# Performance work log

Hardware: AMD Instinct MI355X
Metric: run time of the kernel (lower is better)

Reference implementation:

```python
import jax, jax.numpy as jnp
import numpy as np

B, INP, H, DH = 8192, 2048, 8, 256
HD = H * DH            # 2048
PROJ = int(4 / 3 * HD)  # 2731
EPS = 1e-5


def _layernorm(x, w, b):
    mu = jnp.mean(x, axis=-1, keepdims=True)
    var = jnp.mean((x - mu) ** 2, axis=-1, keepdims=True)
    return (x - mu) * jax.lax.rsqrt(var + EPS) * w + b


def _groupnorm(x, w, b):
    # x: [B, HD] -> groups of size DH (one group per head)
    xg = x.reshape(-1, H, DH)
    mu = jnp.mean(xg, axis=-1, keepdims=True)
    var = jnp.mean((xg - mu) ** 2, axis=-1, keepdims=True)
    xn = ((xg - mu) * jax.lax.rsqrt(var + EPS)).reshape(-1, HD)
    return xn * w + b


def _block_linear(h, R):
    # h: [B, HD], R: [H, DH, DH] block-diagonal recurrent weights (no bias)
    hh = h.reshape(-1, H, DH)
    return jnp.einsum('bhd,hde->bhe', hh, R).reshape(-1, HD)


def setup_inputs() -> dict:
    key = jax.random.key(0)
    ks = jax.random.split(key, 16)
    s = 0.02
    return {
        'seq': jax.random.normal(ks[0], (B, INP), jnp.float32),
        'c_tm1': jnp.zeros((B, HD), jnp.float32),
        'n_tm1': jnp.ones((B, HD), jnp.float32),
        'h_tm1': jnp.zeros((B, HD), jnp.float32),
        'm_tm1': jnp.zeros((B, HD), jnp.float32),
        'ln_w': jnp.ones((INP,), jnp.float32),
        'ln_b': jnp.zeros((INP,), jnp.float32),
        'gn_w': jnp.ones((HD,), jnp.float32),
        'gn_b': jnp.zeros((HD,), jnp.float32),
        'W_i': jax.random.normal(ks[1], (INP, HD), jnp.float32) * s,
        'b_i': jnp.zeros((HD,), jnp.float32),
        'W_f': jax.random.normal(ks[2], (INP, HD), jnp.float32) * s,
        'b_f': jnp.zeros((HD,), jnp.float32),
        'W_z': jax.random.normal(ks[3], (INP, HD), jnp.float32) * s,
        'b_z': jnp.zeros((HD,), jnp.float32),
        'W_o': jax.random.normal(ks[4], (INP, HD), jnp.float32) * s,
        'b_o': jnp.zeros((HD,), jnp.float32),
        'R_i': jax.random.normal(ks[5], (H, DH, DH), jnp.float32) * s,
        'R_f': jax.random.normal(ks[6], (H, DH, DH), jnp.float32) * s,
        'R_z': jax.random.normal(ks[7], (H, DH, DH), jnp.float32) * s,
        'R_o': jax.random.normal(ks[8], (H, DH, DH), jnp.float32) * s,
        'W_up': jax.random.normal(ks[9], (HD, 2 * PROJ), jnp.float32) * s,
        'b_up': jnp.zeros((2 * PROJ,), jnp.float32),
        'W_dn': jax.random.normal(ks[10], (PROJ, INP), jnp.float32) * s,
        'b_dn': jnp.zeros((INP,), jnp.float32),
    }


def reference(seq, c_tm1, n_tm1, h_tm1, m_tm1, ln_w, ln_b, gn_w, gn_b,
              W_i, b_i, W_f, b_f, W_z, b_z, W_o, b_o,
              R_i, R_f, R_z, R_o, W_up, b_up, W_dn, b_dn):
    x_t = _layernorm(seq, ln_w, ln_b)
    x_c = x_t  # use_conv=False path

    i_t = x_c @ W_i + b_i + _block_linear(h_tm1, R_i)
    f_t = x_c @ W_f + b_f + _block_linear(h_tm1, R_f)
    z_t = x_t @ W_z + b_z + _block_linear(h_tm1, R_z)
    o_t = x_t @ W_o + b_o + _block_linear(h_tm1, R_o)

    m_t = jnp.maximum(f_t + m_tm1, i_t)          # stabilizer state
    i_g = jnp.exp(i_t - m_t)
    f_g = jnp.exp(f_t - m_t + m_tm1)
    z_g = jnp.tanh(z_t)
    o_g = jax.nn.sigmoid(o_t)

    c_t = f_g * c_tm1 + i_g * z_g
    n_t = f_g * n_tm1 + i_g
    h_t = o_g * (c_t / n_t)

    out = _groupnorm(h_t, gn_w, gn_b)
    up = out @ W_up + b_up
    out1, out2 = up[:, :PROJ], up[:, PROJ:]
    out = out1 + jax.nn.gelu(out2, approximate=False)
    out = out @ W_dn + b_dn
    return (out + seq, (c_t, n_t, h_t, m_t))
```

## Files before the change

### kernel.cpp

```cpp
#include <hip/hip_runtime.h>
#include <math.h>

typedef unsigned short u16;
typedef __attribute__((ext_vector_type(4))) float f32x4;
typedef __attribute__((ext_vector_type(8))) short bf16x8;
typedef __attribute__((ext_vector_type(8))) unsigned short u16x8;

#define B_ROWS 8192
#define GLDS(gaddr, laddr)                                                                  \
  __builtin_amdgcn_global_load_lds(                                                        \
      (const __attribute__((address_space(1))) unsigned int*)(const void*)(gaddr),          \
      (__attribute__((address_space(3))) unsigned int*)(void*)(laddr), 16, 0, 0)

__device__ __forceinline__ u16 f2bf(float f) {
  unsigned int u = __float_as_uint(f);
  unsigned int r = u + 0x7fffu + ((u >> 16) & 1u);
  return (u16)(r >> 16);
}

__device__ __forceinline__ bf16x8 dsr(unsigned a) {
  bf16x8 d;
  asm volatile("ds_read_b128 %0, %1" : "=v"(d) : "v"(a));
  return d;
}

__device__ __forceinline__ void block_reduce2(float& a, float& b) {
  __shared__ float sb[8];
  #pragma unroll
  for (int off = 32; off > 0; off >>= 1) {
    a += __shfl_down(a, off, 64);
    b += __shfl_down(b, off, 64);
  }
  int lane = threadIdx.x & 63, wid = threadIdx.x >> 6;
  if (lane == 0) { sb[wid] = a; sb[wid + 4] = b; }
  __syncthreads();
  a = sb[0] + sb[1] + sb[2] + sb[3];
  b = sb[4] + sb[5] + sb[6] + sb[7];
  __syncthreads();
}

__global__ __launch_bounds__(256) void ln_kernel(const float* __restrict__ seq,
                                                 const float* __restrict__ w,
                                                 const float* __restrict__ b,
                                                 u16* __restrict__ xbf) {
  int row = blockIdx.x, t = threadIdx.x;
  const f32x4* x = (const f32x4*)(seq + (size_t)row * 2048);
  f32x4 v0 = x[2 * t], v1 = x[2 * t + 1];
  float s = 0.f, q = 0.f;
  #pragma unroll
  for (int i = 0; i < 4; ++i) { s += v0[i] + v1[i]; q += v0[i] * v0[i] + v1[i] * v1[i]; }
  block_reduce2(s, q);
  float mu = s * (1.f / 2048.f);
  float var = q * (1.f / 2048.f) - mu * mu;
  float rstd = rsqrtf(var + 1e-5f);
  f32x4 w0 = ((const f32x4*)w)[2 * t], w1 = ((const f32x4*)w)[2 * t + 1];
  f32x4 b0 = ((const f32x4*)b)[2 * t], b1 = ((const f32x4*)b)[2 * t + 1];
  u16x8 o;
  #pragma unroll
  for (int i = 0; i < 4; ++i) o[i] = f2bf((v0[i] - mu) * rstd * w0[i] + b0[i]);
  #pragma unroll
  for (int i = 0; i < 4; ++i) o[4 + i] = f2bf((v1[i] - mu) * rstd * w1[i] + b1[i]);
  ((u16x8*)(xbf + (size_t)row * 2048))[t] = o;
}

__global__ __launch_bounds__(256) void cvt_bf16(const float* __restrict__ in,
                                                u16* __restrict__ out, int n) {
  int i = blockIdx.x * 256 + threadIdx.x;
  int stride = gridDim.x * 256;
  for (; i < n; i += stride) out[i] = f2bf(in[i]);
}

__global__ void transpose_cvt(const float* __restrict__ in, long ibstride, int R, int Cc,
                              u16* __restrict__ out, long obstride, int ldo) {
  in += (size_t)blockIdx.z * ibstride;
  out += (size_t)blockIdx.z * obstride;
  __shared__ float tile[32][33];
  int c0 = blockIdx.x * 32, r0 = blockIdx.y * 32;
  int tx = threadIdx.x, ty = threadIdx.y;
  #pragma unroll
  for (int j = 0; j < 4; ++j) {
    int rr = r0 + ty + j * 8;
    if (rr < R && c0 + tx < Cc) tile[ty + j * 8][tx] = in[(size_t)rr * Cc + c0 + tx];
  }
  __syncthreads();
  #pragma unroll
  for (int j = 0; j < 4; ++j) {
    int cc = c0 + ty + j * 8, rr = r0 + tx;
    if (cc < Cc && rr < R) out[(size_t)cc * ldo + rr] = f2bf(tile[tx][ty + j * 8]);
  }
}

__global__ __launch_bounds__(256) void pack_bias(const float* __restrict__ bi, const float* __restrict__ bf_,
                                                 const float* __restrict__ bz, const float* __restrict__ bo,
                                                 const float* __restrict__ bup,
                                                 float* __restrict__ biasg, float* __restrict__ biasup) {
  int i = blockIdx.x * 256 + threadIdx.x;
  if (i < 8192) {
    int g = i >> 11, j = i & 2047;
    const float* p = (g == 0) ? bi : (g == 1) ? bf_ : (g == 2) ? bz : bo;
    biasg[i] = p[j];
  }
  if (i < 5504) biasup[i] = (i < 5460) ? bup[i] : 0.f;
}

#define MFMA_CLUSTER(lo, AV, BV)                                                           \
  __builtin_amdgcn_s_setprio(1);                                                           \
  _Pragma("unroll")                                                                        \
  for (int mi = 0; mi < 4; ++mi)                                                           \
    _Pragma("unroll")                                                                      \
    for (int ni = 0; ni < 4; ++ni)                                                         \
      acc[(lo) + mi][ni] =                                                                 \
          __builtin_amdgcn_mfma_f32_16x16x32_bf16(AV[mi], BV[ni], acc[(lo) + mi][ni], 0, 0, 0); \
  __builtin_amdgcn_s_setprio(0);

#define WAIT_LGKM(N)                                                                       \
  asm volatile("s_waitcnt lgkmcnt(" #N ")" ::: "memory");                                  \
  __builtin_amdgcn_sched_barrier(0);

template<int REC>
__global__ __launch_bounds__(512, 2) void gemm256(
    const u16* __restrict__ A, int lda,
    const u16* __restrict__ Bt, int ldb, int KT,
    float* __restrict__ C, long ldc, int Nvalid, int ntN,
    const float* __restrict__ bias,
    const float* __restrict__ addsrc, int ldadd,
    const u16* __restrict__ hbf, const u16* __restrict__ RTw) {
  __shared__ __align__(16) u16 Al[2][2][256][32];
  __shared__ __align__(16) u16 Bl[2][2][256][32];
  const int NT = KT + (REC ? 4 : 0);

  int nb = gridDim.x;
  int bid = blockIdx.x;
  int per = nb >> 3;
  int id = (bid & 7) * per + (bid >> 3);
  int m0 = (id / ntN) * 256, n0 = (id % ntN) * 256;

  int tid = threadIdx.x, lane = tid & 63, wave = tid >> 6;
  int wm = wave >> 2, wn = wave & 3;
  int r = lane & 15, sgrp = lane >> 4;

  const u16* rsrc = nullptr; int hcol = 0;
  if (REC) {
    int g = n0 >> 11, head = (n0 & 2047) >> 8;
    rsrc = RTw + ((size_t)(g * 8 + head)) * 65536;
    hcol = head * 256;
  }

  auto stage = [&](int tt, int which) {
    if (tt >= NT) return;
    const int isA = (which < 2), kh = which & 1, slot = tt & 1;
    const u16* src; size_t ld;
    if (!REC || tt < KT) {
      if (isA) { src = A + (size_t)m0 * lda + tt * 64; ld = lda; }
      else     { src = Bt + (size_t)n0 * ldb + tt * 64; ld = ldb; }
    } else {
      int t2 = tt - KT;
      if (isA) { src = hbf + (size_t)m0 * 2048 + hcol + t2 * 64; ld = 2048; }
      else     { src = rsrc + t2 * 64; ld = 256; }
    }
    u16* base = isA ? &Al[slot][kh][0][0] : &Bl[slot][kh][0][0];
    #pragma unroll
    for (int c = 0; c < 2; ++c) {
      int R0 = wave * 32 + c * 16;
      int row = R0 + (lane >> 2);
      int s = (lane & 3) ^ ((row >> 1) & 3);
      GLDS(src + (size_t)row * ld + kh * 32 + s * 8, base + R0 * 32);
    }
  };

  unsigned AlB = (unsigned)(size_t)(__attribute__((address_space(3))) u16*)&Al[0][0][0][0];
  unsigned BlB = (unsigned)(size_t)(__attribute__((address_space(3))) u16*)&Bl[0][0][0][0];
  int sA = sgrp ^ ((r >> 1) & 3);
  unsigned aBaseT = AlB + (unsigned)((wm * 128 + r) * 64 + sA * 16);
  unsigned bBaseT = BlB + (unsigned)((wn * 64 + r) * 64 + sA * 16);

  f32x4 acc[8][4] = {};
  bf16x8 a0[4], a1[4], a2[4], a3[4], b0[4], b1[4];

  stage(0, 0); stage(0, 2); stage(0, 1); stage(0, 3);
  stage(1, 0); stage(1, 2);
  asm volatile("s_waitcnt vmcnt(4)" ::: "memory");
  __builtin_amdgcn_s_barrier();

  for (int t = 0; t < NT; ++t) {
    unsigned sl = (unsigned)(t & 1) * 32768u;
    unsigned ab = aBaseT + sl, bb = bBaseT + sl;
    __builtin_amdgcn_sched_barrier(0);
    a0[0] = dsr(ab);          a0[1] = dsr(ab + 1024);
    a0[2] = dsr(ab + 2048);   a0[3] = dsr(ab + 3072);
    b0[0] = dsr(bb);          b0[1] = dsr(bb + 1024);
    b0[2] = dsr(bb + 2048);   b0[3] = dsr(bb + 3072);
    a1[0] = dsr(ab + 4096);   a1[1] = dsr(ab + 5120);
    a1[2] = dsr(ab + 6144);   a1[3] = dsr(ab + 7168);
    stage(t + 1, 1); stage(t + 1, 3);
    WAIT_LGKM(4);
    MFMA_CLUSTER(0, a0, b0);
    a2[0] = dsr(ab + 16384);  a2[1] = dsr(ab + 17408);
    a2[2] = dsr(ab + 18432);  a2[3] = dsr(ab + 19456);
    b1[0] = dsr(bb + 16384);  b1[1] = dsr(bb + 17408);
    b1[2] = dsr(bb + 18432);  b1[3] = dsr(bb + 19456);
    WAIT_LGKM(8);
    MFMA_CLUSTER(4, a1, b0);
    __builtin_amdgcn_s_barrier();
    __builtin_amdgcn_sched_barrier(0);
    stage(t + 2, 0); stage(t + 2, 2);
    a3[0] = dsr(ab + 20480);  a3[1] = dsr(ab + 21504);
    a3[2] = dsr(ab + 22528);  a3[3] = dsr(ab + 23552);
    WAIT_LGKM(4);
    MFMA_CLUSTER(0, a2, b1);
    WAIT_LGKM(0);
    MFMA_CLUSTER(4, a3, b1);
    if (t + 2 < NT)      { asm volatile("s_waitcnt vmcnt(4)" ::: "memory"); }
    else if (t + 1 < NT) { asm volatile("s_waitcnt vmcnt(0)" ::: "memory"); }
    __builtin_amdgcn_s_barrier();
  }

  #pragma unroll
  for (int a = 0; a < 8; ++a) {
    int row0 = m0 + wm * 128 + a * 16 + sgrp * 4;
    #pragma unroll
    for (int ni = 0; ni < 4; ++ni) {
      int col = n0 + wn * 64 + ni * 16 + r;
      if (col >= Nvalid) continue;
      float bv = bias ? bias[col] : 0.f;
      #pragma unroll
      for (int jj = 0; jj < 4; ++jj) {
        float v = acc[a][ni][jj] + bv;
        if (addsrc) v += addsrc[(size_t)(row0 + jj) * ldadd + col];
        C[(size_t)(row0 + jj) * ldc + col] = v;
      }
    }
  }
}

__global__ __launch_bounds__(256) void pointwise_gn(
    const float* __restrict__ G, const float* __restrict__ c1, const float* __restrict__ n1,
    const float* __restrict__ m1, const float* __restrict__ gnw, const float* __restrict__ gnb,
    float* __restrict__ outc, float* __restrict__ outn, float* __restrict__ outh,
    float* __restrict__ outm, u16* __restrict__ gnbf) {
  int b = blockIdx.x >> 3, h = blockIdx.x & 7, t = threadIdx.x;
  int j = (h << 8) + t;
  size_t rg = (size_t)b * 8192;
  float it = G[rg + j], ft = G[rg + 2048 + j], zt = G[rg + 4096 + j], ot = G[rg + 6144 + j];
  size_t idx = (size_t)b * 2048 + j;
  float cp = c1[idx], np = n1[idx], mp = m1[idx];
  float mt = fmaxf(ft + mp, it);
  float ig = expf(it - mt), fg = expf(ft - mt + mp);
  float zg = tanhf(zt), og = 1.f / (1.f + expf(-ot));
  float ct = fg * cp + ig * zg;
  float nt = fg * np + ig;
  float ht = og * (ct / nt);
  outc[idx] = ct; outn[idx] = nt; outh[idx] = ht; outm[idx] = mt;
  float s = ht, q = ht * ht;
  block_reduce2(s, q);
  float mu = s * (1.f / 256.f);
  float var = q * (1.f / 256.f) - mu * mu;
  float xn = (ht - mu) * rsqrtf(var + 1e-5f);
  gnbf[idx] = f2bf(xn * gnw[j] + gnb[j]);
}

__global__ __launch_bounds__(256) void act_gelu(const float* __restrict__ tmp, u16* __restrict__ gl) {
  int b = blockIdx.x;
  const float* row = tmp + (size_t)b * 5504;
  u16* orow = gl + (size_t)b * 2752;
  for (int p = threadIdx.x; p < 2752; p += 256) {
    float y = 0.f;
    if (p < 2730) {
      float x1 = row[p], x2 = row[2730 + p];
      y = x1 + x2 * 0.5f * (1.f + erff(x2 * 0.70710678118f));
    }
    orow[p] = f2bf(y);
  }
}

extern "C" void kernel_launch(void* const* d_in, const int* in_sizes, int n_in,
                              void* d_out, int out_size, void* d_ws, size_t ws_size,
                              hipStream_t stream) {
  (void)in_sizes; (void)n_in; (void)out_size; (void)ws_size;
  const float* seq = (const float*)d_in[0];
  const float* c1  = (const float*)d_in[1];
  const float* n1  = (const float*)d_in[2];
  const float* h1  = (const float*)d_in[3];
  const float* m1  = (const float*)d_in[4];
  const float* lnw = (const float*)d_in[5];
  const float* lnb = (const float*)d_in[6];
  const float* gnw = (const float*)d_in[7];
  const float* gnb = (const float*)d_in[8];
  const float* Wi = (const float*)d_in[9];  const float* bi  = (const float*)d_in[10];
  const float* Wf = (const float*)d_in[11]; const float* bf_ = (const float*)d_in[12];
  const float* Wz = (const float*)d_in[13]; const float* bz  = (const float*)d_in[14];
  const float* Wo = (const float*)d_in[15]; const float* bo  = (const float*)d_in[16];
  const float* Ri = (const float*)d_in[17]; const float* Rf = (const float*)d_in[18];
  const float* Rz = (const float*)d_in[19]; const float* Ro = (const float*)d_in[20];
  const float* Wup = (const float*)d_in[21]; const float* bup = (const float*)d_in[22];
  const float* Wdn = (const float*)d_in[23]; const float* bdn = (const float*)d_in[24];

  size_t off = 0;
  char* base = (char*)d_ws;
  auto alloc = [&](size_t bytes) { char* p = base + off; off += (bytes + 255) & ~(size_t)255; return p; };
  u16*   XBF    = (u16*)  alloc((size_t)B_ROWS * 2048 * 2);
  u16*   HBF    = (u16*)  alloc((size_t)B_ROWS * 2048 * 2);
  u16*   WGT    = (u16*)  alloc((size_t)4 * 2048 * 2048 * 2);
  u16*   RT     = (u16*)  alloc((size_t)4 * 8 * 256 * 256 * 2);
  u16*   WUPT   = (u16*)  alloc((size_t)5632 * 2048 * 2);
  u16*   WDNT   = (u16*)  alloc((size_t)2048 * 2752 * 2);
  float* BIASG  = (float*)alloc((size_t)8192 * 4);
  float* BIASUP = (float*)alloc((size_t)5504 * 4);
  u16*   GNBF   = (u16*)  alloc((size_t)B_ROWS * 2048 * 2);
  float* G      = (float*)alloc((size_t)B_ROWS * 8192 * 4);
  float* TMP    = G;
  u16*   GL     = WGT;

  float* OUT  = (float*)d_out;
  float* OUTC = OUT + (size_t)B_ROWS * 2048;
  float* OUTN = OUTC + (size_t)B_ROWS * 2048;
  float* OUTH = OUTN + (size_t)B_ROWS * 2048;
  float* OUTM = OUTH + (size_t)B_ROWS * 2048;

  dim3 tb32(32, 8);

  ln_kernel<<<B_ROWS, 256, 0, stream>>>(seq, lnw, lnb, XBF);
  cvt_bf16<<<2048, 256, 0, stream>>>(h1, HBF, B_ROWS * 2048);
  transpose_cvt<<<dim3(64, 64, 1), tb32, 0, stream>>>(Wi, 0, 2048, 2048, WGT + (size_t)0 * 4194304, 0, 2048);
  transpose_cvt<<<dim3(64, 64, 1), tb32, 0, stream>>>(Wf, 0, 2048, 2048, WGT + (size_t)1 * 4194304, 0, 2048);
  transpose_cvt<<<dim3(64, 64, 1), tb32, 0, stream>>>(Wz, 0, 2048, 2048, WGT + (size_t)2 * 4194304, 0, 2048);
  transpose_cvt<<<dim3(64, 64, 1), tb32, 0, stream>>>(Wo, 0, 2048, 2048, WGT + (size_t)3 * 4194304, 0, 2048);
  transpose_cvt<<<dim3(8, 8, 8), tb32, 0, stream>>>(Ri, 65536, 256, 256, RT + (size_t)0 * 524288, 65536, 256);
  transpose_cvt<<<dim3(8, 8, 8), tb32, 0, stream>>>(Rf, 65536, 256, 256, RT + (size_t)1 * 524288, 65536, 256);
  transpose_cvt<<<dim3(8, 8, 8), tb32, 0, stream>>>(Rz, 65536, 256, 256, RT + (size_t)2 * 524288, 65536, 256);
  transpose_cvt<<<dim3(8, 8, 8), tb32, 0, stream>>>(Ro, 65536, 256, 256, RT + (size_t)3 * 524288, 65536, 256);
  transpose_cvt<<<dim3(171, 64, 1), tb32, 0, stream>>>(Wup, 0, 2048, 5460, WUPT, 0, 2048);
  transpose_cvt<<<dim3(64, 86, 1), tb32, 0, stream>>>(Wdn, 0, 2730, 2048, WDNT, 0, 2752);
  pack_bias<<<32, 256, 0, stream>>>(bi, bf_, bz, bo, bup, BIASG, BIASUP);
  gemm256<1><<<32 * 32, 512, 0, stream>>>(XBF, 2048, WGT, 2048, 32,
                                          G, 8192, 8192, 32, BIASG, nullptr, 0, HBF, RT);
  pointwise_gn<<<B_ROWS * 8, 256, 0, stream>>>(G, c1, n1, m1, gnw, gnb,
                                               OUTC, OUTN, OUTH, OUTM, GNBF);
  gemm256<0><<<32 * 22, 512, 0, stream>>>(GNBF, 2048, WUPT, 2048, 32,
                                          TMP, 5504, 5460, 22, BIASUP, nullptr, 0, nullptr, nullptr);
  act_gelu<<<8192, 256, 0, stream>>>(TMP, GL);
  gemm256<0><<<32 * 8, 512, 0, stream>>>(GL, 2752, WDNT, 2752, 43,
                                         OUT, 2048, 2048, 8, bdn, seq, 2048, nullptr, nullptr);
}
```

Baseline: 1.487 ms.

## Merge prep kernels, store up-proj in bf16, vectorize pointwise, reorder GEMM LDS loads

Combines the layernorm and h-to-bf16 conversion into one launch, and batches the gate and recurrent weight transposes into single launches. The up-projection GEMM now writes bf16 instead of fp32, which halves the intermediate traffic read by the GELU kernel. The pointwise/groupnorm kernel is vectorized to one row per block with wave-level reductions, and the main GEMM loop issues its global staging earlier and batches more LDS reads before the first MFMA cluster. Rounding the up-projection output to bf16 adds some precision loss ahead of GELU.

Result: no change. 1.490 ms (+0.2%).

```diff
diff --git a/kernel.cpp b/kernel.cpp
--- a/kernel.cpp
+++ b/kernel.cpp
@@ -5,6 +5,7 @@
 typedef __attribute__((ext_vector_type(4))) float f32x4;
 typedef __attribute__((ext_vector_type(8))) short bf16x8;
 typedef __attribute__((ext_vector_type(8))) unsigned short u16x8;
+typedef __attribute__((ext_vector_type(4))) unsigned short u16x4;
 
 #define B_ROWS 8192
 #define GLDS(gaddr, laddr)                                                                  \
@@ -16,6 +17,9 @@
   unsigned int u = __float_as_uint(f);
   unsigned int r = u + 0x7fffu + ((u >> 16) & 1u);
   return (u16)(r >> 16);
+}
+__device__ __forceinline__ float bf2f(u16 v) {
+  return __uint_as_float(((unsigned)v) << 16);
 }
 
 __device__ __forceinline__ bf16x8 dsr(unsigned a) {
@@ -39,41 +43,47 @@
   __syncthreads();
 }
 
-__global__ __launch_bounds__(256) void ln_kernel(const float* __restrict__ seq,
-                                                 const float* __restrict__ w,
-                                                 const float* __restrict__ b,
-                                                 u16* __restrict__ xbf) {
-  int row = blockIdx.x, t = threadIdx.x;
-  const f32x4* x = (const f32x4*)(seq + (size_t)row * 2048);
-  f32x4 v0 = x[2 * t], v1 = x[2 * t + 1];
-  float s = 0.f, q = 0.f;
-  #pragma unroll
-  for (int i = 0; i < 4; ++i) { s += v0[i] + v1[i]; q += v0[i] * v0[i] + v1[i] * v1[i]; }
-  block_reduce2(s, q);
-  float mu = s * (1.f / 2048.f);
-  float var = q * (1.f / 2048.f) - mu * mu;
-  float rstd = rsqrtf(var + 1e-5f);
-  f32x4 w0 = ((const f32x4*)w)[2 * t], w1 = ((const f32x4*)w)[2 * t + 1];
-  f32x4 b0 = ((const f32x4*)b)[2 * t], b1 = ((const f32x4*)b)[2 * t + 1];
-  u16x8 o;
-  #pragma unroll
-  for (int i = 0; i < 4; ++i) o[i] = f2bf((v0[i] - mu) * rstd * w0[i] + b0[i]);
-  #pragma unroll
-  for (int i = 0; i < 4; ++i) o[4 + i] = f2bf((v1[i] - mu) * rstd * w1[i] + b1[i]);
-  ((u16x8*)(xbf + (size_t)row * 2048))[t] = o;
-}
-
-__global__ __launch_bounds__(256) void cvt_bf16(const float* __restrict__ in,
-                                                u16* __restrict__ out, int n) {
-  int i = blockIdx.x * 256 + threadIdx.x;
-  int stride = gridDim.x * 256;
-  for (; i < n; i += stride) out[i] = f2bf(in[i]);
-}
-
-__global__ void transpose_cvt(const float* __restrict__ in, long ibstride, int R, int Cc,
-                              u16* __restrict__ out, long obstride, int ldo) {
-  in += (size_t)blockIdx.z * ibstride;
-  out += (size_t)blockIdx.z * obstride;
+__global__ __launch_bounds__(256) void ln_cvt(const float* __restrict__ seq,
+                                              const float* __restrict__ w,
+                                              const float* __restrict__ b,
+                                              u16* __restrict__ xbf,
+                                              const float* __restrict__ h1,
+                                              u16* __restrict__ hbf) {
+  if (blockIdx.x < 8192) {
+    int row = blockIdx.x, t = threadIdx.x;
+    const f32x4* x = (const f32x4*)(seq + (size_t)row * 2048);
+    f32x4 v0 = x[2 * t], v1 = x[2 * t + 1];
+    float s = 0.f, q = 0.f;
+    #pragma unroll
+    for (int i = 0; i < 4; ++i) { s += v0[i] + v1[i]; q += v0[i] * v0[i] + v1[i] * v1[i]; }
+    block_reduce2(s, q);
+    float mu = s * (1.f / 2048.f);
+    float var = q * (1.f / 2048.f) - mu * mu;
+    float rstd = rsqrtf(var + 1e-5f);
+    f32x4 w0 = ((const f32x4*)w)[2 * t], w1 = ((const f32x4*)w)[2 * t + 1];
+    f32x4 b0 = ((const f32x4*)b)[2 * t], b1 = ((const f32x4*)b)[2 * t + 1];
+    u16x8 o;
+    #pragma unroll
+    for (int i = 0; i < 4; ++i) o[i] = f2bf((v0[i] - mu) * rstd * w0[i] + b0[i]);
+    #pragma unroll
+    for (int i = 0; i < 4; ++i) o[4 + i] = f2bf((v1[i] - mu) * rstd * w1[i] + b1[i]);
+    ((u16x8*)(xbf + (size_t)row * 2048))[t] = o;
+  } else {
+    int chunk = blockIdx.x - 8192;
+    const f32x4* src = (const f32x4*)(h1 + (size_t)chunk * 8192);
+    u16x8* dst = (u16x8*)(hbf + (size_t)chunk * 8192);
+    for (int i = threadIdx.x; i < 1024; i += 256) {
+      f32x4 v0 = src[2 * i], v1 = src[2 * i + 1];
+      u16x8 o;
+      #pragma unroll
+      for (int j = 0; j < 4; ++j) { o[j] = f2bf(v0[j]); o[4 + j] = f2bf(v1[j]); }
+      dst[i] = o;
+    }
+  }
+}
+
+__device__ __forceinline__ void tr_tile(const float* in, int R, int Cc,
+                                        u16* out, int ldo) {
   __shared__ float tile[32][33];
   int c0 = blockIdx.x * 32, r0 = blockIdx.y * 32;
   int tx = threadIdx.x, ty = threadIdx.y;
@@ -88,6 +98,27 @@
     int cc = c0 + ty + j * 8, rr = r0 + tx;
     if (cc < Cc && rr < R) out[(size_t)cc * ldo + rr] = f2bf(tile[tx][ty + j * 8]);
   }
+}
+
+__global__ void transpose_cvt(const float* __restrict__ in, int R, int Cc,
+                              u16* __restrict__ out, int ldo) {
+  tr_tile(in, R, Cc, out, ldo);
+}
+
+__global__ void transpose_gate4(const float* __restrict__ W0, const float* __restrict__ W1,
+                                const float* __restrict__ W2, const float* __restrict__ W3,
+                                u16* __restrict__ out) {
+  int z = blockIdx.z;
+  const float* in = (z == 0) ? W0 : (z == 1) ? W1 : (z == 2) ? W2 : W3;
+  tr_tile(in, 2048, 2048, out + (size_t)z * 4194304, 2048);
+}
+
+__global__ void transpose_rec4(const float* __restrict__ R0, const float* __restrict__ R1,
+                               const float* __restrict__ R2, const float* __restrict__ R3,
+                               u16* __restrict__ out) {
+  int g = blockIdx.z >> 3, hd = blockIdx.z & 7;
+  const float* in = ((g == 0) ? R0 : (g == 1) ? R1 : (g == 2) ? R2 : R3) + (size_t)hd * 65536;
+  tr_tile(in, 256, 256, out + (size_t)g * 524288 + (size_t)hd * 65536, 256);
 }
 
 __global__ __launch_bounds__(256) void pack_bias(const float* __restrict__ bi, const float* __restrict__ bf_,
@@ -117,11 +148,11 @@
   asm volatile("s_waitcnt lgkmcnt(" #N ")" ::: "memory");                                  \
   __builtin_amdgcn_sched_barrier(0);
 
-template<int REC>
+template<int REC, int OB>
 __global__ __launch_bounds__(512, 2) void gemm256(
     const u16* __restrict__ A, int lda,
     const u16* __restrict__ Bt, int ldb, int KT,
-    float* __restrict__ C, long ldc, int Nvalid, int ntN,
+    void* __restrict__ Cv, long ldc, int Nvalid, int ntN,
     const float* __restrict__ bias,
     const float* __restrict__ addsrc, int ldadd,
     const u16* __restrict__ hbf, const u16* __restrict__ RTw) {
@@ -186,19 +217,19 @@
     unsigned sl = (unsigned)(t & 1) * 32768u;
     unsigned ab = aBaseT + sl, bb = bBaseT + sl;
     __builtin_amdgcn_sched_barrier(0);
+    stage(t + 1, 1); stage(t + 1, 3);
     a0[0] = dsr(ab);          a0[1] = dsr(ab + 1024);
     a0[2] = dsr(ab + 2048);   a0[3] = dsr(ab + 3072);
     b0[0] = dsr(bb);          b0[1] = dsr(bb + 1024);
     b0[2] = dsr(bb + 2048);   b0[3] = dsr(bb + 3072);
     a1[0] = dsr(ab + 4096);   a1[1] = dsr(ab + 5120);
     a1[2] = dsr(ab + 6144);   a1[3] = dsr(ab + 7168);
-    stage(t + 1, 1); stage(t + 1, 3);
-    WAIT_LGKM(4);
-    MFMA_CLUSTER(0, a0, b0);
     a2[0] = dsr(ab + 16384);  a2[1] = dsr(ab + 17408);
     a2[2] = dsr(ab + 18432);  a2[3] = dsr(ab + 19456);
     b1[0] = dsr(bb + 16384);  b1[1] = dsr(bb + 17408);
     b1[2] = dsr(bb + 18432);  b1[3] = dsr(bb + 19456);
+    WAIT_LGKM(12);
+    MFMA_CLUSTER(0, a0, b0);
     WAIT_LGKM(8);
     MFMA_CLUSTER(4, a1, b0);
     __builtin_amdgcn_s_barrier();
@@ -227,49 +258,76 @@
       for (int jj = 0; jj < 4; ++jj) {
         float v = acc[a][ni][jj] + bv;
         if (addsrc) v += addsrc[(size_t)(row0 + jj) * ldadd + col];
-        C[(size_t)(row0 + jj) * ldc + col] = v;
+        if (OB) ((u16*)Cv)[(size_t)(row0 + jj) * ldc + col] = f2bf(v);
+        else    ((float*)Cv)[(size_t)(row0 + jj) * ldc + col] = v;
       }
     }
   }
 }
 
-__global__ __launch_bounds__(256) void pointwise_gn(
+__global__ __launch_bounds__(512) void pointwise_gn(
     const float* __restrict__ G, const float* __restrict__ c1, const float* __restrict__ n1,
     const float* __restrict__ m1, const float* __restrict__ gnw, const float* __restrict__ gnb,
     float* __restrict__ outc, float* __restrict__ outn, float* __restrict__ outh,
     float* __restrict__ outm, u16* __restrict__ gnbf) {
-  int b = blockIdx.x >> 3, h = blockIdx.x & 7, t = threadIdx.x;
-  int j = (h << 8) + t;
+  int b = blockIdx.x;
+  int w = threadIdx.x >> 6, l = threadIdx.x & 63;
+  int j = (w << 8) + l * 4;
   size_t rg = (size_t)b * 8192;
-  float it = G[rg + j], ft = G[rg + 2048 + j], zt = G[rg + 4096 + j], ot = G[rg + 6144 + j];
+  f32x4 it = *(const f32x4*)(G + rg + j);
+  f32x4 ft = *(const f32x4*)(G + rg + 2048 + j);
+  f32x4 zt = *(const f32x4*)(G + rg + 4096 + j);
+  f32x4 ot = *(const f32x4*)(G + rg + 6144 + j);
   size_t idx = (size_t)b * 2048 + j;
-  float cp = c1[idx], np = n1[idx], mp = m1[idx];
-  float mt = fmaxf(ft + mp, it);
-  float ig = expf(it - mt), fg = expf(ft - mt + mp);
-  float zg = tanhf(zt), og = 1.f / (1.f + expf(-ot));
-  float ct = fg * cp + ig * zg;
-  float nt = fg * np + ig;
-  float ht = og * (ct / nt);
-  outc[idx] = ct; outn[idx] = nt; outh[idx] = ht; outm[idx] = mt;
-  float s = ht, q = ht * ht;
-  block_reduce2(s, q);
+  f32x4 cp = *(const f32x4*)(c1 + idx);
+  f32x4 np = *(const f32x4*)(n1 + idx);
+  f32x4 mp = *(const f32x4*)(m1 + idx);
+  f32x4 ct, nt, ht, mt;
+  float s = 0.f, q = 0.f;
+  #pragma unroll
+  for (int i = 0; i < 4; ++i) {
+    float m_ = fmaxf(ft[i] + mp[i], it[i]);
+    float ig = expf(it[i] - m_), fg = expf(ft[i] - m_ + mp[i]);
+    float zg = tanhf(zt[i]), og = 1.f / (1.f + expf(-ot[i]));
+    ct[i] = fg * cp[i] + ig * zg;
+    nt[i] = fg * np[i] + ig;
+    ht[i] = og * (ct[i] / nt[i]);
+    mt[i] = m_;
+    s += ht[i]; q += ht[i] * ht[i];
+  }
+  *(f32x4*)(outc + idx) = ct;
+  *(f32x4*)(outn + idx) = nt;
+  *(f32x4*)(outh + idx) = ht;
+  *(f32x4*)(outm + idx) = mt;
+  #pragma unroll
+  for (int off = 32; off > 0; off >>= 1) {
+    s += __shfl_xor(s, off, 64);
+    q += __shfl_xor(q, off, 64);
+  }
   float mu = s * (1.f / 256.f);
   float var = q * (1.f / 256.f) - mu * mu;
-  float xn = (ht - mu) * rsqrtf(var + 1e-5f);
-  gnbf[idx] = f2bf(xn * gnw[j] + gnb[j]);
-}
-
-__global__ __launch_bounds__(256) void act_gelu(const float* __restrict__ tmp, u16* __restrict__ gl) {
+  float rs = rsqrtf(var + 1e-5f);
+  f32x4 gw = *(const f32x4*)(gnw + j), gb = *(const f32x4*)(gnb + j);
+  u16x4 o;
+  #pragma unroll
+  for (int i = 0; i < 4; ++i) o[i] = f2bf((ht[i] - mu) * rs * gw[i] + gb[i]);
+  *(u16x4*)(gnbf + idx) = o;
+}
+
+__global__ __launch_bounds__(256) void act_gelu(const u16* __restrict__ tmp, u16* __restrict__ gl) {
   int b = blockIdx.x;
-  const float* row = tmp + (size_t)b * 5504;
+  const u16* row = tmp + (size_t)b * 5504;
   u16* orow = gl + (size_t)b * 2752;
-  for (int p = threadIdx.x; p < 2752; p += 256) {
-    float y = 0.f;
+  for (int p = threadIdx.x * 2; p < 2752; p += 512) {
+    float y0 = 0.f, y1 = 0.f;
     if (p < 2730) {
-      float x1 = row[p], x2 = row[2730 + p];
-      y = x1 + x2 * 0.5f * (1.f + erff(x2 * 0.70710678118f));
-    }
-    orow[p] = f2bf(y);
+      float x10 = bf2f(row[p]), x11 = bf2f(row[p + 1]);
+      float x20 = bf2f(row[2730 + p]), x21 = bf2f(row[2731 + p]);
+      y0 = x10 + x20 * 0.5f * (1.f + erff(x20 * 0.70710678118f));
+      y1 = x11 + x21 * 0.5f * (1.f + erff(x21 * 0.70710678118f));
+    }
+    orow[p] = f2bf(y0);
+    orow[p + 1] = f2bf(y1);
   }
 }
 
@@ -308,7 +366,7 @@
   float* BIASUP = (float*)alloc((size_t)5504 * 4);
   u16*   GNBF   = (u16*)  alloc((size_t)B_ROWS * 2048 * 2);
   float* G      = (float*)alloc((size_t)B_ROWS * 8192 * 4);
-  float* TMP    = G;
+  u16*   TMP    = (u16*)G;
   u16*   GL     = WGT;
 
   float* OUT  = (float*)d_out;
@@ -319,26 +377,19 @@
 
   dim3 tb32(32, 8);
 
-  ln_kernel<<<B_ROWS, 256, 0, stream>>>(seq, lnw, lnb, XBF);
-  cvt_bf16<<<2048, 256, 0, stream>>>(h1, HBF, B_ROWS * 2048);
-  transpose_cvt<<<dim3(64, 64, 1), tb32, 0, stream>>>(Wi, 0, 2048, 2048, WGT + (size_t)0 * 4194304, 0, 2048);
-  transpose_cvt<<<dim3(64, 64, 1), tb32, 0, stream>>>(Wf, 0, 2048, 2048, WGT + (size_t)1 * 4194304, 0, 2048);
-  transpose_cvt<<<dim3(64, 64, 1), tb32, 0, stream>>>(Wz, 0, 2048, 2048, WGT + (size_t)2 * 4194304, 0, 2048);
-  transpose_cvt<<<dim3(64, 64, 1), tb32, 0, stream>>>(Wo, 0, 2048, 2048, WGT + (size_t)3 * 4194304, 0, 2048);
-  transpose_cvt<<<dim3(8, 8, 8), tb32, 0, stream>>>(Ri, 65536, 256, 256, RT + (size_t)0 * 524288, 65536, 256);
-  transpose_cvt<<<dim3(8, 8, 8), tb32, 0, stream>>>(Rf, 65536, 256, 256, RT + (size_t)1 * 524288, 65536, 256);
-  transpose_cvt<<<dim3(8, 8, 8), tb32, 0, stream>>>(Rz, 65536, 256, 256, RT + (size_t)2 * 524288, 65536, 256);
-  transpose_cvt<<<dim3(8, 8, 8), tb32, 0, stream>>>(Ro, 65536, 256, 256, RT + (size_t)3 * 524288, 65536, 256);
-  transpose_cvt<<<dim3(171, 64, 1), tb32, 0, stream>>>(Wup, 0, 2048, 5460, WUPT, 0, 2048);
-  transpose_cvt<<<dim3(64, 86, 1), tb32, 0, stream>>>(Wdn, 0, 2730, 2048, WDNT, 0, 2752);
+  ln_cvt<<<8192 + 2048, 256, 0, stream>>>(seq, lnw, lnb, XBF, h1, HBF);
+  transpose_gate4<<<dim3(64, 64, 4), tb32, 0, stream>>>(Wi, Wf, Wz, Wo, WGT);
+  transpose_rec4<<<dim3(8, 8, 32), tb32, 0, stream>>>(Ri, Rf, Rz, Ro, RT);
+  transpose_cvt<<<dim3(171, 64, 1), tb32, 0, stream>>>(Wup, 2048, 5460, WUPT, 2048);
+  transpose_cvt<<<dim3(64, 86, 1), tb32, 0, stream>>>(Wdn, 2730, 2048, WDNT, 2752);
   pack_bias<<<32, 256, 0, stream>>>(bi, bf_, bz, bo, bup, BIASG, BIASUP);
-  gemm256<1><<<32 * 32, 512, 0, stream>>>(XBF, 2048, WGT, 2048, 32,
-                                          G, 8192, 8192, 32, BIASG, nullptr, 0, HBF, RT);
-  pointwise_gn<<<B_ROWS * 8, 256, 0, stream>>>(G, c1, n1, m1, gnw, gnb,
-                                               OUTC, OUTN, OUTH, OUTM, GNBF);
-  gemm256<0><<<32 * 22, 512, 0, stream>>>(GNBF, 2048, WUPT, 2048, 32,
-                                          TMP, 5504, 5460, 22, BIASUP, nullptr, 0, nullptr, nullptr);
+  gemm256<1, 0><<<32 * 32, 512, 0, stream>>>(XBF, 2048, WGT, 2048, 32,
+                                             G, 8192, 8192, 32, BIASG, nullptr, 0, HBF, RT);
+  pointwise_gn<<<B_ROWS, 512, 0, stream>>>(G, c1, n1, m1, gnw, gnb,
+                                           OUTC, OUTN, OUTH, OUTM, GNBF);
+  gemm256<0, 1><<<32 * 22, 512, 0, stream>>>(GNBF, 2048, WUPT, 2048, 32,
+                                             TMP, 5504, 5460, 22, BIASUP, nullptr, 0, nullptr, nullptr);
   act_gelu<<<8192, 256, 0, stream>>>(TMP, GL);
-  gemm256<0><<<32 * 8, 512, 0, stream>>>(GL, 2752, WDNT, 2752, 43,
-                                         OUT, 2048, 2048, 8, bdn, seq, 2048, nullptr, nullptr);
-}
+  gemm256<0, 0><<<32 * 8, 512, 0, stream>>>(GL, 2752, WDNT, 2752, 43,
+                                            OUT, 2048, 2048, 8, bdn, seq, 2048, nullptr, nullptr);
+}
```
